# Performance work log

Hardware: AMD Instinct MI355X
Metric: run time of the kernel (lower is better)

Reference implementation:

```python
import jax, jax.numpy as jnp
import numpy as np

B, CIN, HIN, WIN = 8192, 16, 6, 6
FM = 64                      # feature_maps
DK = FM // 2                 # 32
DV = FM // 2                 # 32
NH = FM // 2                 # 32 heads -> dkh = dvh = 1
OUT_CH = 5
HID = 128


def _conv2d(x, w, b, stride=1):
    # x: NCHW, w: OIHW, VALID padding (padding=(k-1)//2 = 0 for k=2)
    y = jax.lax.conv_general_dilated(
        x, w, window_strides=(stride, stride), padding='VALID',
        dimension_numbers=('NCHW', 'OIHW', 'NCHW'))
    return y + b[None, :, None, None]


def setup_inputs() -> dict:
    key = jax.random.key(0)
    ks = jax.random.split(key, 13)
    s = 0.1  # small init scale keeps softmax logits well-conditioned
    return {
        'x':      jax.random.normal(ks[0], (B, CIN, HIN, WIN), jnp.float32),
        # AugmentedConv: conv_out (out_channels - dv), qkv conv (2dk+dv), attn 1x1
        'conv_w': jax.random.normal(ks[1], (FM - DV, CIN, 2, 2), jnp.float32) * s,
        'conv_b': jax.random.normal(ks[2], (FM - DV,), jnp.float32) * s,
        'qkv_w':  jax.random.normal(ks[3], (2 * DK + DV, CIN, 2, 2), jnp.float32) * s,
        'qkv_b':  jax.random.normal(ks[4], (2 * DK + DV,), jnp.float32) * s,
        'attn_w': jax.random.normal(ks[5], (DV, DV, 1, 1), jnp.float32) * s,
        'attn_b': jax.random.normal(ks[6], (DV,), jnp.float32) * s,
        # DoubleDense: fm*5*5 -> hid -> hid//2 -> out
        'w1': jax.random.normal(ks[7], (HID, FM * 5 * 5), jnp.float32) * s,
        'b1': jax.random.normal(ks[8], (HID,), jnp.float32) * s,
        'w2': jax.random.normal(ks[9], (HID // 2, HID), jnp.float32) * s,
        'b2': jax.random.normal(ks[10], (HID // 2,), jnp.float32) * s,
        'w3': jax.random.normal(ks[11], (OUT_CH, HID // 2), jnp.float32) * s,
        'b3': jax.random.normal(ks[12], (OUT_CH,), jnp.float32) * s,
    }


def _forward(x, conv_w, conv_b, qkv_w, qkv_b, attn_w, attn_b, w1, b1, w2, b2, w3, b3):
    # ---- AugmentedConv ----
    conv_out = _conv2d(x, conv_w, conv_b)            # [B, FM-DV, 5, 5]
    qkv = _conv2d(x, qkv_w, qkv_b)                   # [B, 2DK+DV, 5, 5]
    b, _, h, w = qkv.shape
    q, k, v = jnp.split(qkv, [DK, 2 * DK], axis=1)
    dkh = DK // NH
    q = q * (dkh ** -0.5)
    flat_q = q.reshape(b, NH, dkh, h * w)            # [B, Nh, dkh, HW]
    flat_k = k.reshape(b, NH, dkh, h * w)
    flat_v = v.reshape(b, NH, DV // NH, h * w)
    # logits = q^T k over head-dim: [B, Nh, HW, HW]
    logits = jnp.einsum('bndi,bndj->bnij', flat_q, flat_k)
    weights = jax.nn.softmax(logits, axis=-1)
    # attn = weights @ v^T -> [B, Nh, HW, dvh]
    attn = jnp.einsum('bnij,bnjd->bnid', weights, flat_v.transpose(0, 1, 3, 2))
    # faithful to torch: raw reshape (B, Nh, dvh, H, W) then combine heads
    attn = attn.reshape(b, NH, DV // NH, h, w).reshape(b, DV, h, w)
    attn = _conv2d(attn, attn_w, attn_b)             # 1x1 conv
    y = jnp.concatenate([conv_out, attn], axis=1)    # [B, FM, 5, 5]
    # ---- ReLU + DoubleDense ----
    y = jax.nn.relu(y).reshape(b, -1)                # [B, FM*25]
    y = jax.nn.relu(y @ w1.T + b1)
    y = jax.nn.relu(y @ w2.T + b2)
    return y @ w3.T + b3                             # [B, OUT_CH]


def reference(x, conv_w, conv_b, qkv_w, qkv_b, attn_w, attn_b, w1, b1, w2, b2, w3, b3):
    return _forward(x, conv_w, conv_b, qkv_w, qkv_b, attn_w, attn_b,
                    w1, b1, w2, b2, w3, b3)
```

## Files before the change

### kernel.cpp

```cpp
#include <hip/hip_runtime.h>
#include <hip/hip_bf16.h>
#include <cstdint>
#include <cstddef>


typedef __attribute__((ext_vector_type(4))) float f32x4;
typedef __attribute__((ext_vector_type(8))) __bf16 bf16x8;
typedef __attribute__((ext_vector_type(4))) __bf16 bf16x4;

#define LOG2E 1.4426950408889634f

__device__ __forceinline__ float fast_exp2(float x) {
#if __has_builtin(__builtin_amdgcn_exp2f)
  return __builtin_amdgcn_exp2f(x);
#else
  return __expf(x * 0.6931471805599453f);
#endif
}

__device__ __forceinline__ f32x4 mfma16(bf16x8 a, bf16x8 b, f32x4 c) {
  return __builtin_amdgcn_mfma_f32_16x16x32_bf16(a, b, c, 0, 0, 0);
}

__global__ __launch_bounds__(256) void prep(
    const float* __restrict__ conv_w, const float* __restrict__ conv_b,
    const float* __restrict__ qkv_w,  const float* __restrict__ qkv_b,
    const float* __restrict__ w1, const float* __restrict__ w2,
    __hip_bfloat16* __restrict__ wqb, __hip_bfloat16* __restrict__ w1bp,
    __hip_bfloat16* __restrict__ w2b, float* __restrict__ biasb) {
  int i = blockIdx.x * 256 + threadIdx.x;
  if (i < 128 * 1600) {
    int n = i / 1600, r = i - n * 1600;
    int c = r & 63, p = r >> 6;
    w1bp[i] = __float2bfloat16(w1[n * 1600 + c * 25 + p]);
  }
  if (i < 8192) {
    float w = (i < 2048) ? conv_w[i] : qkv_w[i - 2048];
    if (i >= 4096 && i < 6144) w *= LOG2E;
    wqb[i] = __float2bfloat16(w);
    w2b[i] = __float2bfloat16(w2[i]);
  }
  if (i < 128) {
    float b = (i < 32) ? conv_b[i] : qkv_b[i - 32];
    if (i >= 64 && i < 96) b *= LOG2E;
    biasb[i] = b;
  }
}

__global__ __launch_bounds__(256) void k1(
    const float* __restrict__ x,
    const float* __restrict__ biasb,
    const __hip_bfloat16* __restrict__ wqb,
    const float* __restrict__ attn_w, const float* __restrict__ attn_b,
    __hip_bfloat16* __restrict__ act) {
  const int t = threadIdx.x;
  const int lane = t & 63, wave = t >> 6;
  const int l15 = lane & 15, quad = lane >> 4;
  const int b0 = blockIdx.x * 4;

  __shared__ __align__(16) char lds_raw[6400 + 21504];
  __bf16* xs  = (__bf16*)lds_raw;
  __bf16* as_ = (__bf16*)lds_raw;
  __bf16* qs  = (__bf16*)(lds_raw + 6400);

  const float* xb = x + (size_t)b0 * 576;
#pragma unroll
  for (int i = 0; i < 9; ++i) {
    int f = t + i * 256;
    xs[f] = __float2bfloat16(xb[f]);
  }

  bf16x8 bfr[8][2];
#pragma unroll
  for (int nt = 0; nt < 8; ++nt)
#pragma unroll
    for (int ks = 0; ks < 2; ++ks)
      bfr[nt][ks] = *(const bf16x8*)((const __bf16*)wqb + (nt * 16 + l15) * 64 + ks * 32 + quad * 8);
  float bias[8];
#pragma unroll
  for (int nt = 0; nt < 8; ++nt) bias[nt] = biasb[nt * 16 + l15];
  __syncthreads();

  for (int mt = wave; mt < 7; mt += 4) {
    int row = mt * 16 + l15;
    int rc = row < 99 ? row : 99;
    int bl = rc / 25, pos = rc - bl * 25;
    int ii = pos / 5, jj = pos - ii * 5;
    const __bf16* xp = xs + bl * 576 + ii * 6 + jj;
    bf16x8 af[2];
#pragma unroll
    for (int ks = 0; ks < 2; ++ks) {
      const __bf16* p0 = xp + (ks * 8 + quad * 2) * 36;
      bf16x8 a;
      a[0] = p0[0];  a[1] = p0[1];  a[2] = p0[6];  a[3] = p0[7];
      a[4] = p0[36]; a[5] = p0[37]; a[6] = p0[42]; a[7] = p0[43];
      af[ks] = a;
    }
    f32x4 acc[8];
#pragma unroll
    for (int nt = 0; nt < 8; ++nt) acc[nt] = (f32x4){0.f, 0.f, 0.f, 0.f};
#pragma unroll
    for (int ks = 0; ks < 2; ++ks)
#pragma unroll
      for (int nt = 0; nt < 8; ++nt)
        acc[nt] = mfma16(af[ks], bfr[nt][ks], acc[nt]);

#pragma unroll
    for (int r = 0; r < 4; ++r) {
      int orow = mt * 16 + quad * 4 + r;
      if (orow < 100) {
        int ob = orow / 25, op = orow - ob * 25;
#pragma unroll
        for (int nt = 0; nt < 8; ++nt) {
          float v = acc[nt][r] + bias[nt];
          if (nt < 2) {
            act[((size_t)(b0 + ob) * 25 + op) * 64 + nt * 16 + l15] =
                __float2bfloat16(fmaxf(v, 0.f));
          } else {
            qs[(ob * 96 + (nt - 2) * 16 + l15) * 28 + op] = __float2bfloat16(v);
          }
        }
      }
    }
  }
  __syncthreads();

  {
    const int pair = t & 127, half = t >> 7;
    const int bl = pair >> 5, n = pair & 31;
    const __bf16* qp = qs + (bl * 96 + n) * 28;
    const __bf16* kp = qp + 32 * 28;
    const __bf16* vp = qp + 64 * 28;
    float kl[25], vv[25];
#pragma unroll
    for (int c4 = 0; c4 < 6; ++c4) {
      bf16x4 b = *(const bf16x4*)(kp + c4 * 4);
      bf16x4 c = *(const bf16x4*)(vp + c4 * 4);
#pragma unroll
      for (int z = 0; z < 4; ++z) {
        kl[c4 * 4 + z] = (float)b[z];
        vv[c4 * 4 + z] = (float)c[z];
      }
    }
    kl[24] = (float)kp[24]; vv[24] = (float)vp[24];

    const int i0 = half * 12;
    float qv[13];
    {
      const __bf16* qbase = qp + i0;
      bf16x4 q0 = *(const bf16x4*)(qbase);
      bf16x4 q1 = *(const bf16x4*)(qbase + 4);
      bf16x4 q2 = *(const bf16x4*)(qbase + 8);
#pragma unroll
      for (int z = 0; z < 4; ++z) {
        qv[z] = (float)q0[z]; qv[4 + z] = (float)q1[z]; qv[8 + z] = (float)q2[z];
      }
      qv[12] = (float)qbase[12];
    }

#pragma unroll
    for (int z = 0; z < 13; ++z) {
      const float qi = qv[z];
      float s0 = 0.f, s1 = 0.f, s2 = 0.f, s3 = 0.f, s4 = 0.f;
      float o0 = 0.f, o1 = 0.f, o2 = 0.f, o3 = 0.f, o4 = 0.f;
#pragma unroll
      for (int g = 0; g < 5; ++g) {
        float e0 = fast_exp2(qi * kl[g * 5 + 0]);
        float e1 = fast_exp2(qi * kl[g * 5 + 1]);
        float e2 = fast_exp2(qi * kl[g * 5 + 2]);
        float e3 = fast_exp2(qi * kl[g * 5 + 3]);
        float e4 = fast_exp2(qi * kl[g * 5 + 4]);
        s0 += e0; o0 = __builtin_fmaf(e0, vv[g * 5 + 0], o0);
        s1 += e1; o1 = __builtin_fmaf(e1, vv[g * 5 + 1], o1);
        s2 += e2; o2 = __builtin_fmaf(e2, vv[g * 5 + 2], o2);
        s3 += e3; o3 = __builtin_fmaf(e3, vv[g * 5 + 3], o3);
        s4 += e4; o4 = __builtin_fmaf(e4, vv[g * 5 + 4], o4);
      }
      float ss = ((s0 + s1) + (s2 + s3)) + s4;
      float oo = ((o0 + o1) + (o2 + o3)) + o4;
      as_[(bl * 25 + i0 + z) * 32 + n] = __float2bfloat16(oo * __builtin_amdgcn_rcpf(ss));
    }
  }
  __syncthreads();

  {
    bf16x8 bw[2]; float ab[2];
#pragma unroll
    for (int nt2 = 0; nt2 < 2; ++nt2) {
      int n = nt2 * 16 + l15;
#pragma unroll
      for (int j = 0; j < 8; ++j)
        bw[nt2][j] = (__bf16)__float2bfloat16(attn_w[n * 32 + quad * 8 + j]);
      ab[nt2] = attn_b[n];
    }
    for (int mt = wave; mt < 7; mt += 4) {
      int row = mt * 16 + l15;
      int rc = row < 99 ? row : 99;
      bf16x8 af = *(const bf16x8*)(as_ + rc * 32 + quad * 8);
      f32x4 acc[2];
#pragma unroll
      for (int nt2 = 0; nt2 < 2; ++nt2)
        acc[nt2] = mfma16(af, bw[nt2], (f32x4){0.f, 0.f, 0.f, 0.f});
#pragma unroll
      for (int r = 0; r < 4; ++r) {
        int orow = mt * 16 + quad * 4 + r;
        if (orow < 100) {
          int ob = orow / 25, op = orow - ob * 25;
#pragma unroll
          for (int nt2 = 0; nt2 < 2; ++nt2)
            act[((size_t)(b0 + ob) * 25 + op) * 64 + 32 + nt2 * 16 + l15] =
                __float2bfloat16(fmaxf(acc[nt2][r] + ab[nt2], 0.f));
        }
      }
    }
  }
}

__global__ __launch_bounds__(512) void k2(
    const __hip_bfloat16* __restrict__ act,
    const __hip_bfloat16* __restrict__ w1bp, const float* __restrict__ b1,
    const __hip_bfloat16* __restrict__ w2b, const float* __restrict__ b2,
    const float* __restrict__ w3, const float* __restrict__ b3,
    float* __restrict__ out) {
  const int t = threadIdx.x;
  const int lane = t & 63;
  const int wave = t >> 6;
  const int wm = wave >> 2;
  const int wn = wave & 3;
  const int l15 = lane & 15;
  const int quad = lane >> 4;
  const int b0 = blockIdx.x * 32;

  __shared__ __hip_bfloat16 C1s[32 * 136];
  __shared__ __hip_bfloat16 C2s[32 * 72];

  f32x4 acc0 = {0.f, 0.f, 0.f, 0.f};
  f32x4 acc1 = {0.f, 0.f, 0.f, 0.f};
  const __bf16* aptr  = (const __bf16*)act + (size_t)(b0 + wm * 16 + l15) * 1600 + quad * 8;
  const __bf16* bptr0 = (const __bf16*)w1bp + (size_t)(wn * 32 + l15) * 1600 + quad * 8;
  const __bf16* bptr1 = bptr0 + 16 * 1600;
#pragma unroll 5
  for (int k0 = 0; k0 < 1600; k0 += 32) {
    bf16x8 av  = *(const bf16x8*)(aptr + k0);
    bf16x8 bv0 = *(const bf16x8*)(bptr0 + k0);
    bf16x8 bv1 = *(const bf16x8*)(bptr1 + k0);
    acc0 = mfma16(av, bv0, acc0);
    acc1 = mfma16(av, bv1, acc1);
  }
  {
    const int col0 = wn * 32 + l15;
    const float bias0 = b1[col0];
    const float bias1 = b1[col0 + 16];
#pragma unroll
    for (int r = 0; r < 4; ++r) {
      const int row = wm * 16 + quad * 4 + r;
      C1s[row * 136 + col0]      = __float2bfloat16(fmaxf(acc0[r] + bias0, 0.f));
      C1s[row * 136 + col0 + 16] = __float2bfloat16(fmaxf(acc1[r] + bias1, 0.f));
    }
  }
  __syncthreads();

  f32x4 acc2 = {0.f, 0.f, 0.f, 0.f};
  {
    const __bf16* aL = (const __bf16*)C1s + (wm * 16 + l15) * 136 + quad * 8;
    const __bf16* bL = (const __bf16*)w2b + (wn * 16 + l15) * 128 + quad * 8;
#pragma unroll
    for (int k0 = 0; k0 < 128; k0 += 32)
      acc2 = mfma16(*(const bf16x8*)(aL + k0), *(const bf16x8*)(bL + k0), acc2);
  }
  {
    const int col = wn * 16 + l15;
    const float bias = b2[col];
#pragma unroll
    for (int r = 0; r < 4; ++r) {
      const int row = wm * 16 + quad * 4 + r;
      C2s[row * 72 + col] = __float2bfloat16(fmaxf(acc2[r] + bias, 0.f));
    }
  }
  __syncthreads();

  if (t < 160) {
    const int row = t / 5;
    const int oc = t - row * 5;
    float s = b3[oc];
#pragma unroll
    for (int k = 0; k < 64; ++k)
      s += __bfloat162float(C2s[row * 72 + k]) * w3[oc * 64 + k];
    out[(size_t)(b0 + row) * 5 + oc] = s;
  }
}

extern "C" void kernel_launch(void* const* d_in, const int* in_sizes, int n_in,
                              void* d_out, int out_size, void* d_ws, size_t ws_size,
                              hipStream_t stream) {
  const float* x      = (const float*)d_in[0];
  const float* conv_w = (const float*)d_in[1];
  const float* conv_b = (const float*)d_in[2];
  const float* qkv_w  = (const float*)d_in[3];
  const float* qkv_b  = (const float*)d_in[4];
  const float* attn_w = (const float*)d_in[5];
  const float* attn_b = (const float*)d_in[6];
  const float* w1 = (const float*)d_in[7];
  const float* b1 = (const float*)d_in[8];
  const float* w2 = (const float*)d_in[9];
  const float* b2 = (const float*)d_in[10];
  const float* w3 = (const float*)d_in[11];
  const float* b3 = (const float*)d_in[12];
  float* out = (float*)d_out;

  char* ws = (char*)d_ws;
  __hip_bfloat16* act  = (__hip_bfloat16*)ws;
  __hip_bfloat16* w1bp = (__hip_bfloat16*)(ws + 26214400);
  __hip_bfloat16* w2b  = (__hip_bfloat16*)(ws + 26624000);
  __hip_bfloat16* wqb  = (__hip_bfloat16*)(ws + 26640384);
  float*          biasb = (float*)(ws + 26656768);

  prep<<<dim3(800), dim3(256), 0, stream>>>(conv_w, conv_b, qkv_w, qkv_b,
                                            w1, w2, wqb, w1bp, w2b, biasb);
  k1<<<dim3(2048), dim3(256), 0, stream>>>(x, biasb, wqb, attn_w, attn_b, act);
  k2<<<dim3(256), dim3(512), 0, stream>>>(act, w1bp, b1, w2b, b2, w3, b3, out);
}
```

Baseline: 178.2 us.

## Run attention-conv kernel with one single-wave block per sample, no barriers

The conv+attention kernel now uses one 64-thread block per batch sample instead of 256 threads covering four samples. With a single wave, the block-wide barriers between the conv, attention and projection stages are removed. This also replaces the uneven split of 7 MFMA row tiles across 4 waves with 2 tiles per wave. Separately, attn_w is converted to bf16 once in the prep kernel, so each block loads it as vectors instead of converting per element. The cost is more padding waste in the 16-row tiles (25 rows padded to 32) and a 4x larger grid. Correctness now relies on LDS ordering within a single wave.

```diff
diff --git a/kernel.cpp b/kernel.cpp
--- a/kernel.cpp
+++ b/kernel.cpp
@@ -25,9 +25,11 @@
 __global__ __launch_bounds__(256) void prep(
     const float* __restrict__ conv_w, const float* __restrict__ conv_b,
     const float* __restrict__ qkv_w,  const float* __restrict__ qkv_b,
+    const float* __restrict__ attn_w,
     const float* __restrict__ w1, const float* __restrict__ w2,
     __hip_bfloat16* __restrict__ wqb, __hip_bfloat16* __restrict__ w1bp,
-    __hip_bfloat16* __restrict__ w2b, float* __restrict__ biasb) {
+    __hip_bfloat16* __restrict__ w2b, float* __restrict__ biasb,
+    __hip_bfloat16* __restrict__ wab) {
   int i = blockIdx.x * 256 + threadIdx.x;
   if (i < 128 * 1600) {
     int n = i / 1600, r = i - n * 1600;
@@ -40,6 +42,7 @@
     wqb[i] = __float2bfloat16(w);
     w2b[i] = __float2bfloat16(w2[i]);
   }
+  if (i < 1024) wab[i] = __float2bfloat16(attn_w[i]);
   if (i < 128) {
     float b = (i < 32) ? conv_b[i] : qkv_b[i - 32];
     if (i >= 64 && i < 96) b *= LOG2E;
@@ -47,26 +50,25 @@
   }
 }
 
-__global__ __launch_bounds__(256) void k1(
+__global__ __launch_bounds__(64) void k1(
     const float* __restrict__ x,
     const float* __restrict__ biasb,
     const __hip_bfloat16* __restrict__ wqb,
-    const float* __restrict__ attn_w, const float* __restrict__ attn_b,
+    const __hip_bfloat16* __restrict__ wab, const float* __restrict__ attn_b,
     __hip_bfloat16* __restrict__ act) {
   const int t = threadIdx.x;
-  const int lane = t & 63, wave = t >> 6;
-  const int l15 = lane & 15, quad = lane >> 4;
-  const int b0 = blockIdx.x * 4;
-
-  __shared__ __align__(16) char lds_raw[6400 + 21504];
+  const int l15 = t & 15, quad = t >> 4;
+  const int b = blockIdx.x;
+
+  __shared__ __align__(16) char lds_raw[1600 + 5376];
   __bf16* xs  = (__bf16*)lds_raw;
   __bf16* as_ = (__bf16*)lds_raw;
-  __bf16* qs  = (__bf16*)(lds_raw + 6400);
-
-  const float* xb = x + (size_t)b0 * 576;
+  __bf16* qs  = (__bf16*)(lds_raw + 1600);
+
+  const float* xb = x + (size_t)b * 576;
 #pragma unroll
   for (int i = 0; i < 9; ++i) {
-    int f = t + i * 256;
+    int f = t + i * 64;
     xs[f] = __float2bfloat16(xb[f]);
   }
 
@@ -79,14 +81,13 @@
   float bias[8];
 #pragma unroll
   for (int nt = 0; nt < 8; ++nt) bias[nt] = biasb[nt * 16 + l15];
-  __syncthreads();
-
-  for (int mt = wave; mt < 7; mt += 4) {
+
+#pragma unroll
+  for (int mt = 0; mt < 2; ++mt) {
     int row = mt * 16 + l15;
-    int rc = row < 99 ? row : 99;
-    int bl = rc / 25, pos = rc - bl * 25;
+    int pos = row < 24 ? row : 24;
     int ii = pos / 5, jj = pos - ii * 5;
-    const __bf16* xp = xs + bl * 576 + ii * 6 + jj;
+    const __bf16* xp = xs + ii * 6 + jj;
     bf16x8 af[2];
 #pragma unroll
     for (int ks = 0; ks < 2; ++ks) {
@@ -108,38 +109,35 @@
 #pragma unroll
     for (int r = 0; r < 4; ++r) {
       int orow = mt * 16 + quad * 4 + r;
-      if (orow < 100) {
-        int ob = orow / 25, op = orow - ob * 25;
+      if (orow < 25) {
 #pragma unroll
         for (int nt = 0; nt < 8; ++nt) {
           float v = acc[nt][r] + bias[nt];
           if (nt < 2) {
-            act[((size_t)(b0 + ob) * 25 + op) * 64 + nt * 16 + l15] =
+            act[((size_t)b * 25 + orow) * 64 + nt * 16 + l15] =
                 __float2bfloat16(fmaxf(v, 0.f));
           } else {
-            qs[(ob * 96 + (nt - 2) * 16 + l15) * 28 + op] = __float2bfloat16(v);
+            qs[((nt - 2) * 16 + l15) * 28 + orow] = __float2bfloat16(v);
           }
         }
       }
     }
   }
-  __syncthreads();
-
-  {
-    const int pair = t & 127, half = t >> 7;
-    const int bl = pair >> 5, n = pair & 31;
-    const __bf16* qp = qs + (bl * 96 + n) * 28;
-    const __bf16* kp = qp + 32 * 28;
-    const __bf16* vp = qp + 64 * 28;
+
+  {
+    const int n = t & 31, half = t >> 5;
+    const __bf16* qp = qs + n * 28;
+    const __bf16* kp = qs + (32 + n) * 28;
+    const __bf16* vp = qs + (64 + n) * 28;
     float kl[25], vv[25];
 #pragma unroll
     for (int c4 = 0; c4 < 6; ++c4) {
-      bf16x4 b = *(const bf16x4*)(kp + c4 * 4);
-      bf16x4 c = *(const bf16x4*)(vp + c4 * 4);
+      bf16x4 bb = *(const bf16x4*)(kp + c4 * 4);
+      bf16x4 cc = *(const bf16x4*)(vp + c4 * 4);
 #pragma unroll
       for (int z = 0; z < 4; ++z) {
-        kl[c4 * 4 + z] = (float)b[z];
-        vv[c4 * 4 + z] = (float)c[z];
+        kl[c4 * 4 + z] = (float)bb[z];
+        vv[c4 * 4 + z] = (float)cc[z];
       }
     }
     kl[24] = (float)kp[24]; vv[24] = (float)vp[24];
@@ -178,24 +176,22 @@
       }
       float ss = ((s0 + s1) + (s2 + s3)) + s4;
       float oo = ((o0 + o1) + (o2 + o3)) + o4;
-      as_[(bl * 25 + i0 + z) * 32 + n] = __float2bfloat16(oo * __builtin_amdgcn_rcpf(ss));
-    }
-  }
-  __syncthreads();
+      as_[(i0 + z) * 32 + n] = __float2bfloat16(oo * __builtin_amdgcn_rcpf(ss));
+    }
+  }
 
   {
     bf16x8 bw[2]; float ab[2];
 #pragma unroll
     for (int nt2 = 0; nt2 < 2; ++nt2) {
       int n = nt2 * 16 + l15;
-#pragma unroll
-      for (int j = 0; j < 8; ++j)
-        bw[nt2][j] = (__bf16)__float2bfloat16(attn_w[n * 32 + quad * 8 + j]);
+      bw[nt2] = *(const bf16x8*)((const __bf16*)wab + n * 32 + quad * 8);
       ab[nt2] = attn_b[n];
     }
-    for (int mt = wave; mt < 7; mt += 4) {
+#pragma unroll
+    for (int mt = 0; mt < 2; ++mt) {
       int row = mt * 16 + l15;
-      int rc = row < 99 ? row : 99;
+      int rc = row < 24 ? row : 24;
       bf16x8 af = *(const bf16x8*)(as_ + rc * 32 + quad * 8);
       f32x4 acc[2];
 #pragma unroll
@@ -204,11 +200,10 @@
 #pragma unroll
       for (int r = 0; r < 4; ++r) {
         int orow = mt * 16 + quad * 4 + r;
-        if (orow < 100) {
-          int ob = orow / 25, op = orow - ob * 25;
+        if (orow < 25) {
 #pragma unroll
           for (int nt2 = 0; nt2 < 2; ++nt2)
-            act[((size_t)(b0 + ob) * 25 + op) * 64 + 32 + nt2 * 16 + l15] =
+            act[((size_t)b * 25 + orow) * 64 + 32 + nt2 * 16 + l15] =
                 __float2bfloat16(fmaxf(acc[nt2][r] + ab[nt2], 0.f));
         }
       }
@@ -309,14 +304,15 @@
   float* out = (float*)d_out;
 
   char* ws = (char*)d_ws;
-  __hip_bfloat16* act  = (__hip_bfloat16*)ws;
-  __hip_bfloat16* w1bp = (__hip_bfloat16*)(ws + 26214400);
-  __hip_bfloat16* w2b  = (__hip_bfloat16*)(ws + 26624000);
-  __hip_bfloat16* wqb  = (__hip_bfloat16*)(ws + 26640384);
+  __hip_bfloat16* act   = (__hip_bfloat16*)ws;
+  __hip_bfloat16* w1bp  = (__hip_bfloat16*)(ws + 26214400);
+  __hip_bfloat16* w2b   = (__hip_bfloat16*)(ws + 26624000);
+  __hip_bfloat16* wqb   = (__hip_bfloat16*)(ws + 26640384);
   float*          biasb = (float*)(ws + 26656768);
-
-  prep<<<dim3(800), dim3(256), 0, stream>>>(conv_w, conv_b, qkv_w, qkv_b,
-                                            w1, w2, wqb, w1bp, w2b, biasb);
-  k1<<<dim3(2048), dim3(256), 0, stream>>>(x, biasb, wqb, attn_w, attn_b, act);
+  __hip_bfloat16* wab   = (__hip_bfloat16*)(ws + 26657280);
+
+  prep<<<dim3(800), dim3(256), 0, stream>>>(conv_w, conv_b, qkv_w, qkv_b, attn_w,
+                                            w1, w2, wqb, w1bp, w2b, biasb, wab);
+  k1<<<dim3(8192), dim3(64), 0, stream>>>(x, biasb, wqb, wab, attn_b, act);
   k2<<<dim3(256), dim3(512), 0, stream>>>(act, w1bp, b1, w2b, b2, w3, b3, out);
 }
```

Measured after the change: 173.0 us. 2.9% less time.
